# Performance work log

Measured on AMD Instinct MI355X. Metric: run time of the kernel, lower is better.

The kernel has to match this reference:

```python
import jax, jax.numpy as jnp
import numpy as np

N = 50000   # nodes
E = 800000  # edges
F = 128     # n_features
H = 128     # n_hidden
LN_EPS = 1e-5


def setup_inputs() -> dict:
    key = jax.random.key(0)
    ks = jax.random.split(key, 11)
    s = 0.05
    return {
        "x": jax.random.normal(ks[0], (N, F), jnp.float32),
        "edge_index": jax.random.randint(ks[1], (2, E), 0, N, dtype=jnp.int64),
        "edge_attr": jax.random.uniform(ks[2], (E, 1), jnp.float32),
        "ln_gamma": jax.random.normal(ks[3], (F,), jnp.float32),
        "ln_beta": jax.random.normal(ks[4], (F,), jnp.float32),
        "W1": jax.random.normal(ks[5], (F, H), jnp.float32) * s,
        "b1": jax.random.normal(ks[6], (H,), jnp.float32) * s,
        "W2": jax.random.normal(ks[7], (H, H), jnp.float32) * s,
        "b2": jax.random.normal(ks[8], (H,), jnp.float32) * s,
        "W3": jax.random.normal(ks[9], (H, 1), jnp.float32) * s,
        "b3": jax.random.normal(ks[10], (1,), jnp.float32) * s,
    }


def _gcn_conv(x, W, b, row, col, ew, n_nodes):
    """PyG GCNConv: add self loops (weight 1), symmetric normalization,
    gather-scale-scatter aggregation, linear (no bias) + bias."""
    loop = jnp.arange(n_nodes, dtype=row.dtype)
    row_f = jnp.concatenate([row, loop])          # [E+N] source
    col_f = jnp.concatenate([col, loop])          # [E+N] target
    ew_f = jnp.concatenate([ew, jnp.ones((n_nodes,), ew.dtype)])
    deg = jax.ops.segment_sum(ew_f, col_f, num_segments=n_nodes)  # [N]
    dis = jnp.where(deg > 0, jax.lax.rsqrt(jnp.where(deg > 0, deg, 1.0)), 0.0)
    norm = dis[row_f] * ew_f * dis[col_f]          # [E+N]
    h = x @ W                                      # [N, out]
    msg = h[row_f] * norm[:, None]                 # [E+N, out] gather+scale
    out = jax.ops.segment_sum(msg, col_f, num_segments=n_nodes)  # scatter-add
    return out + b


def reference(x, edge_index, edge_attr, ln_gamma, ln_beta, W1, b1, W2, b2, W3, b3):
    x = jnp.nan_to_num(x, nan=0.0, posinf=0.0, neginf=0.0)
    ew = jnp.nan_to_num(edge_attr[:, 0], nan=0.0, posinf=1.0, neginf=0.0)  # [E]
    row, col = edge_index[0], edge_index[1]
    # input LayerNorm
    mu = jnp.mean(x, axis=-1, keepdims=True)
    var = jnp.mean(jnp.square(x - mu), axis=-1, keepdims=True)
    x = (x - mu) * jax.lax.rsqrt(var + LN_EPS) * ln_gamma + ln_beta
    # hidden GCN layers (dropout = identity in eval mode)
    x = jax.nn.relu(_gcn_conv(x, W1, b1, row, col, ew, N))
    x = jax.nn.relu(_gcn_conv(x, W2, b2, row, col, ew, N))
    # output layer
    return _gcn_conv(x, W3, b3, row, col, ew, N)  # [N, 1]
```

## Files before the change

kernel.cpp:

```cpp
#include <hip/hip_runtime.h>
#include <hip/hip_fp16.h>
#include <math.h>

#define NNODES 50000
#define NEDGES 800000
#define NF 128
#define BK 64
#define BINSH 7
#define BINS ((NNODES + 127) >> BINSH)
#define BINCAP 2560
#define EPT 8
#define EPB (1024 * EPT)
constexpr float LN_EPS = 1e-5f;

typedef short v8s __attribute__((ext_vector_type(8)));
typedef unsigned short v8u __attribute__((ext_vector_type(8)));
typedef float v4f __attribute__((ext_vector_type(4)));

__device__ __forceinline__ float clean0(float v) {
    return (isnan(v) || isinf(v)) ? 0.0f : v;
}
__device__ __forceinline__ float cleanw(float v) {
    if (isnan(v)) return 0.0f;
    if (isinf(v)) return v > 0.0f ? 1.0f : 0.0f;
    return v;
}
__device__ __forceinline__ int clampN(int v) {
    return min(max(v, 0), NNODES - 1);
}
__device__ __forceinline__ int pad8(int v) { return (v + 7) & ~7; }

__device__ __forceinline__ unsigned short f2bf(float f) {
    unsigned int u = __float_as_uint(f);
    return (unsigned short)((u + 0x7FFFu + ((u >> 16) & 1u)) >> 16);
}
__device__ __forceinline__ float bf2f(unsigned short h) {
    return __uint_as_float(((unsigned int)h) << 16);
}
__device__ __forceinline__ void split_bf(float v, unsigned short& h, unsigned short& l) {
    h = f2bf(v);
    l = f2bf(v - bf2f(h));
}

__global__ __launch_bounds__(1024) void k_bin_ln(
        const int* __restrict__ ei, const float* __restrict__ ea,
        int* __restrict__ gbin, int2* __restrict__ binned,
        const float* __restrict__ x, const float* __restrict__ gamma,
        const float* __restrict__ beta, unsigned short* __restrict__ z,
        int nbe) {
    if ((int)blockIdx.x < nbe) {
        __shared__ int lcnt[BINS];
        __shared__ int lbase[BINS];
        for (int i = threadIdx.x; i < BINS; i += 1024) lcnt[i] = 0;
        __syncthreads();
        int e0 = blockIdx.x * EPB + threadIdx.x;
        int   myb[EPT]; int myr[EPT]; int mysrc[EPT]; float myw[EPT];
        #pragma unroll
        for (int j = 0; j < EPT; j++) {
            int e = e0 + j * 1024;
            myb[j] = -1;
            if (e < NEDGES) {
                int r = clampN(ei[e]);
                int c = clampN(ei[NEDGES + e]);
                float w = cleanw(ea[e]);
                int b = c >> BINSH;
                myb[j] = b;
                mysrc[j] = ((c & 127) << 16) | r;
                myw[j] = w;
                myr[j] = atomicAdd(&lcnt[b], 1);
            }
        }
        __syncthreads();
        for (int i = threadIdx.x; i < BINS; i += 1024)
            if (lcnt[i] > 0) lbase[i] = atomicAdd(&gbin[i], lcnt[i]);
        __syncthreads();
        #pragma unroll
        for (int j = 0; j < EPT; j++) {
            if (myb[j] >= 0) {
                int pos = lbase[myb[j]] + myr[j];
                if (pos < BINCAP)
                    binned[(size_t)myb[j] * BINCAP + pos] =
                        make_int2(mysrc[j], __float_as_int(myw[j]));
            }
        }
    } else {
        int bid = blockIdx.x - nbe;
        int n = (bid * 1024 + threadIdx.x) >> 6;
        int lane = threadIdx.x & 63;
        if (n >= NNODES) return;
        float2 v = ((const float2*)(x + (size_t)n * NF))[lane];
        v.x = clean0(v.x); v.y = clean0(v.y);
        float s = v.x + v.y;
        for (int o = 32; o > 0; o >>= 1) s += __shfl_xor(s, o);
        float mu = s * (1.0f / NF);
        float dx = v.x - mu, dy = v.y - mu;
        float q = dx * dx + dy * dy;
        for (int o = 32; o > 0; o >>= 1) q += __shfl_xor(q, o);
        float rstd = rsqrtf(q * (1.0f / NF) + LN_EPS);
        float2 g = ((const float2*)gamma)[lane];
        float b = ((const float2*)beta)[lane].x;
        float b2v = ((const float2*)beta)[lane].y;
        float ox = dx * rstd * g.x + b;
        float oy = dy * rstd * g.y + b2v;
        ((__half2*)z)[(size_t)n * 64 + lane] = __float22half2_rn(make_float2(ox, oy));
    }
}

__global__ __launch_bounds__(1024) void k_bucketize(
        const int2* __restrict__ binned, const int* __restrict__ gbin,
        int2* __restrict__ bucket, int* __restrict__ cnt, float* __restrict__ dis,
        const float* __restrict__ W1, const float* __restrict__ W2,
        unsigned short* __restrict__ Wh1T, unsigned short* __restrict__ Wl1T,
        unsigned short* __restrict__ Wh2T, unsigned short* __restrict__ Wl2T,
        int nbb) {
    if ((int)blockIdx.x < nbb) {
        __shared__ int   lc[128];
        __shared__ float ld[128];
        int b = blockIdx.x;
        if (threadIdx.x < 128) { lc[threadIdx.x] = 0; ld[threadIdx.x] = 1.0f; }
        __syncthreads();
        int tot = min(gbin[b], BINCAP);
        const int2* src = binned + (size_t)b * BINCAP;
        for (int i = threadIdx.x; i < tot; i += 1024) {
            int2 rec = src[i];
            int dlo = (rec.x >> 16) & 127;
            int s = rec.x & 0xFFFF;
            int pos = atomicAdd(&lc[dlo], 1);
            int n = (b << BINSH) + dlo;
            if (pos < BK) bucket[(n << 6) + pos] = make_int2(s, rec.y);
            atomicAdd(&ld[dlo], __int_as_float(rec.y));
        }
        __syncthreads();
        if (threadIdx.x < 128) {
            int n = (b << BINSH) + threadIdx.x;
            if (n < NNODES) {
                int c = min(lc[threadIdx.x], BK);
                int cp = pad8(c);
                int beg = n << 6;
                for (int p = beg + c; p < beg + cp; p++) bucket[p] = make_int2(0, 0);
                cnt[n] = cp;
                dis[n] = rsqrtf(ld[threadIdx.x]);
            }
        }
    } else {
        int idx = (blockIdx.x - nbb) * 1024 + threadIdx.x;
        int m = idx >> 14;
        int n = (idx >> 7) & 127;
        int k = idx & 127;
        const float* W = m ? W2 : W1;
        unsigned short* Wh = m ? Wh2T : Wh1T;
        unsigned short* Wl = m ? Wl2T : Wl1T;
        unsigned short h, l;
        split_bf(W[k * 128 + n], h, l);
        Wh[n * 128 + k] = h;
        Wl[n * 128 + k] = l;
    }
}

__global__ __launch_bounds__(256) void k_gemm_mfma(
        const unsigned short* __restrict__ Ain,
        const unsigned short* __restrict__ BhT, const unsigned short* __restrict__ BlT,
        const float* __restrict__ dis, unsigned short* __restrict__ C) {
    int w = threadIdx.x >> 6;
    int lane = threadIdx.x & 63;
    int m = lane & 15;
    int q = lane >> 4;
    int rowbase = blockIdx.x * 64 + w * 16;
    int arow = min(rowbase + m, NNODES - 1);

    const v8u* ap = (const v8u*)(Ain + (size_t)arow * NF);
    v8s afh[4], afl[4];
    #pragma unroll
    for (int c = 0; c < 4; c++) {
        v8u a = ap[c * 4 + q];
        #pragma unroll
        for (int j = 0; j < 8; j++) {
            float f = __half2float(__ushort_as_half(a[j]));
            unsigned short hh, ll;
            split_bf(f, hh, ll);
            afh[c][j] = (short)hh;
            afl[c][j] = (short)ll;
        }
    }

    float ds[4];
    #pragma unroll
    for (int r = 0; r < 4; r++) ds[r] = dis[min(rowbase + q * 4 + r, NNODES - 1)];

    for (int nt = 0; nt < 8; nt++) {
        int n0 = nt * 16;
        const v8s* bhp = (const v8s*)(BhT + (size_t)(n0 + m) * NF);
        const v8s* blp = (const v8s*)(BlT + (size_t)(n0 + m) * NF);
        v4f acc = {0.f, 0.f, 0.f, 0.f};
        #pragma unroll
        for (int c = 0; c < 4; c++) {
            v8s bh = bhp[c * 4 + q];
            v8s bl = blp[c * 4 + q];
            acc = __builtin_amdgcn_mfma_f32_16x16x32_bf16(afh[c], bh, acc, 0, 0, 0);
            acc = __builtin_amdgcn_mfma_f32_16x16x32_bf16(afh[c], bl, acc, 0, 0, 0);
            acc = __builtin_amdgcn_mfma_f32_16x16x32_bf16(afl[c], bh, acc, 0, 0, 0);
        }
        #pragma unroll
        for (int r = 0; r < 4; r++) {
            int gr = rowbase + q * 4 + r;
            if (gr < NNODES)
                C[(size_t)gr * NF + n0 + m] = __half_as_ushort(__float2half(acc[r] * ds[r]));
        }
    }
}

template <bool LAST>
__global__ __launch_bounds__(256) void k_aggregate(
        const unsigned short* __restrict__ h, const float* __restrict__ dis,
        const int* __restrict__ cntp, const int2* __restrict__ bucket,
        const float* __restrict__ bias, unsigned short* __restrict__ y,
        const float* __restrict__ W3, float* __restrict__ h3) {
    int n0 = (blockIdx.x * blockDim.x + threadIdx.x) >> 6;
    if (n0 >= NNODES) return;
    int n = __builtin_amdgcn_readfirstlane(n0);
    int lane = threadIdx.x & 63;
    const __half2* hp = (const __half2*)h;
    float2 acc = __half22float2(hp[(size_t)n * 64 + lane]);
    int beg = n << 6;
    int end = beg + cntp[n];
    int p = beg;
    if (p < end) {
        int2 rec[8];
        #pragma unroll
        for (int j = 0; j < 8; j++) rec[j] = bucket[p + j];
        p += 8;
        while (p < end) {
            float2 v[8];
            #pragma unroll
            for (int j = 0; j < 8; j++) v[j] = __half22float2(hp[(size_t)rec[j].x * 64 + lane]);
            int2 rec2[8];
            #pragma unroll
            for (int j = 0; j < 8; j++) rec2[j] = bucket[p + j];
            #pragma unroll
            for (int j = 0; j < 8; j++) {
                float w = __int_as_float(rec[j].y);
                acc.x += v[j].x * w;
                acc.y += v[j].y * w;
            }
            #pragma unroll
            for (int j = 0; j < 8; j++) rec[j] = rec2[j];
            p += 8;
        }
        float2 v[8];
        #pragma unroll
        for (int j = 0; j < 8; j++) v[j] = __half22float2(hp[(size_t)rec[j].x * 64 + lane]);
        #pragma unroll
        for (int j = 0; j < 8; j++) {
            float w = __int_as_float(rec[j].y);
            acc.x += v[j].x * w;
            acc.y += v[j].y * w;
        }
    }
    float dn = dis[n];
    float2 b = ((const float2*)bias)[lane];
    float ox = fmaxf(acc.x * dn + b.x, 0.0f);
    float oy = fmaxf(acc.y * dn + b.y, 0.0f);
    if (LAST) {
        float2 w3 = ((const float2*)W3)[lane];
        float s = ox * w3.x + oy * w3.y;
        for (int o = 32; o > 0; o >>= 1) s += __shfl_xor(s, o);
        if (lane == 0) h3[n] = s * dn;
    } else {
        ((__half2*)y)[(size_t)n * 64 + lane] = __float22half2_rn(make_float2(ox, oy));
    }
}

__global__ void k_agg_scalar(const float* __restrict__ h3, const float* __restrict__ dis,
                             const int* __restrict__ cntp, const int2* __restrict__ bucket,
                             const float* __restrict__ b3, float* __restrict__ out) {
    int n = blockIdx.x * blockDim.x + threadIdx.x;
    if (n >= NNODES) return;
    float acc = h3[n];
    int beg = n << 6;
    int end = beg + cntp[n];
    for (int p = beg; p + 4 <= end; p += 4) {
        int2 e0 = bucket[p], e1 = bucket[p + 1], e2 = bucket[p + 2], e3 = bucket[p + 3];
        float v0 = h3[e0.x], v1 = h3[e1.x], v2 = h3[e2.x], v3 = h3[e3.x];
        acc += v0 * __int_as_float(e0.y) + v1 * __int_as_float(e1.y)
             + v2 * __int_as_float(e2.y) + v3 * __int_as_float(e3.y);
    }
    out[n] = acc * dis[n] + b3[0];
}

extern "C" void kernel_launch(void* const* d_in, const int* in_sizes, int n_in,
                              void* d_out, int out_size, void* d_ws, size_t ws_size,
                              hipStream_t stream) {
    const float* x  = (const float*)d_in[0];
    const int*   ei = (const int*)d_in[1];
    const float* ea = (const float*)d_in[2];
    const float* g  = (const float*)d_in[3];
    const float* be = (const float*)d_in[4];
    const float* W1 = (const float*)d_in[5];
    const float* b1 = (const float*)d_in[6];
    const float* W2 = (const float*)d_in[7];
    const float* b2 = (const float*)d_in[8];
    const float* W3 = (const float*)d_in[9];
    const float* b3 = (const float*)d_in[10];
    float* out = (float*)d_out;

    char* ws = (char*)d_ws;
    size_t off = 0;
    auto alloc = [&](size_t bytes) {
        void* p = ws + off;
        off += (bytes + 255) & ~((size_t)255);
        return p;
    };
    unsigned short* zbuf = (unsigned short*)alloc((size_t)NNODES * NF * 2);
    unsigned short* hbuf = (unsigned short*)alloc((size_t)NNODES * NF * 2);
    float* dis    = (float*)alloc((size_t)NNODES * 4);
    int*   cnt    = (int*)  alloc((size_t)NNODES * 4);
    int2*  bucket = (int2*) alloc((size_t)NNODES * BK * 8);
    float* h3     = (float*)alloc((size_t)NNODES * 4);
    unsigned short* Wh1T = (unsigned short*)alloc(128 * 128 * 2);
    unsigned short* Wl1T = (unsigned short*)alloc(128 * 128 * 2);
    unsigned short* Wh2T = (unsigned short*)alloc(128 * 128 * 2);
    unsigned short* Wl2T = (unsigned short*)alloc(128 * 128 * 2);
    int*  gbin   = (int*) alloc((size_t)BINS * 4);
    int2* binned = (int2*)alloc((size_t)BINS * BINCAP * 8);
    (void)ws_size; (void)in_sizes; (void)n_in; (void)out_size;

    const int NB_N  = (NNODES + 255) / 256;
    const int NB_W  = (NNODES * 64 + 255) / 256;
    const int NB_G  = (NNODES + 63) / 64;
    const int NBE   = (NEDGES + EPB - 1) / EPB;
    const int NB_LN = NNODES * 64 / 1024;

    hipMemsetAsync(gbin, 0, (size_t)BINS * 4, stream);
    k_bin_ln<<<NBE + NB_LN, 1024, 0, stream>>>(ei, ea, gbin, binned,
                                               x, g, be, zbuf, NBE);
    k_bucketize<<<BINS + 32, 1024, 0, stream>>>(binned, gbin, bucket, cnt, dis,
                                                W1, W2, Wh1T, Wl1T, Wh2T, Wl2T, BINS);

    k_gemm_mfma<<<NB_G, 256, 0, stream>>>(zbuf, Wh1T, Wl1T, dis, hbuf);
    k_aggregate<false><<<NB_W, 256, 0, stream>>>(hbuf, dis, cnt, bucket, b1, zbuf,
                                                 nullptr, nullptr);
    k_gemm_mfma<<<NB_G, 256, 0, stream>>>(zbuf, Wh2T, Wl2T, dis, hbuf);
    k_aggregate<true><<<NB_W, 256, 0, stream>>>(hbuf, dis, cnt, bucket, b2, nullptr,
                                                W3, h3);
    k_agg_scalar<<<NB_N, 256, 0, stream>>>(h3, dis, cnt, bucket, b3, out);
}
```

Baseline: 252.5 us.

## Use fp16 MFMA GEMM and split each wave across two edges in aggregation

The GEMM stops converting the fp16 activations into split bf16 hi/lo pairs. It now feeds fp16 A directly into fp16 MFMA against fp16 hi/lo weight splits, which drops from three MFMAs per k-chunk to two and removes the per-element conversion work. The aggregation kernel now has each half-wave handle a different edge, with each lane loading 8 bytes (4 halves) instead of 4. The two halves are combined with a cross-lane shuffle at the end, which widens memory transactions and halves the serial edge loop. The trade-off is lower A precision in the GEMM (fp16 only, no lo part) and extra shuffle and reduction work in aggregation.

```diff
diff --git a/kernel.cpp b/kernel.cpp
--- a/kernel.cpp
+++ b/kernel.cpp
@@ -13,8 +13,7 @@
 #define EPB (1024 * EPT)
 constexpr float LN_EPS = 1e-5f;
 
-typedef short v8s __attribute__((ext_vector_type(8)));
-typedef unsigned short v8u __attribute__((ext_vector_type(8)));
+typedef _Float16 v8h __attribute__((ext_vector_type(8)));
 typedef float v4f __attribute__((ext_vector_type(4)));
 
 __device__ __forceinline__ float clean0(float v) {
@@ -30,16 +29,13 @@
 }
 __device__ __forceinline__ int pad8(int v) { return (v + 7) & ~7; }
 
-__device__ __forceinline__ unsigned short f2bf(float f) {
-    unsigned int u = __float_as_uint(f);
-    return (unsigned short)((u + 0x7FFFu + ((u >> 16) & 1u)) >> 16);
-}
-__device__ __forceinline__ float bf2f(unsigned short h) {
-    return __uint_as_float(((unsigned int)h) << 16);
-}
-__device__ __forceinline__ void split_bf(float v, unsigned short& h, unsigned short& l) {
-    h = f2bf(v);
-    l = f2bf(v - bf2f(h));
+__device__ __forceinline__ float2 h2f(unsigned int u) {
+    __half2 h = *reinterpret_cast<__half2*>(&u);
+    return __half22float2(h);
+}
+__device__ __forceinline__ unsigned int f2h2(float a, float b) {
+    __half2 h = __float22half2_rn(make_float2(a, b));
+    return *reinterpret_cast<unsigned int*>(&h);
 }
 
 __global__ __launch_bounds__(1024) void k_bin_ln(
@@ -98,11 +94,10 @@
         for (int o = 32; o > 0; o >>= 1) q += __shfl_xor(q, o);
         float rstd = rsqrtf(q * (1.0f / NF) + LN_EPS);
         float2 g = ((const float2*)gamma)[lane];
-        float b = ((const float2*)beta)[lane].x;
-        float b2v = ((const float2*)beta)[lane].y;
-        float ox = dx * rstd * g.x + b;
-        float oy = dy * rstd * g.y + b2v;
-        ((__half2*)z)[(size_t)n * 64 + lane] = __float22half2_rn(make_float2(ox, oy));
+        float2 bb = ((const float2*)beta)[lane];
+        float ox = dx * rstd * g.x + bb.x;
+        float oy = dy * rstd * g.y + bb.y;
+        ((unsigned int*)z)[(size_t)n * 64 + lane] = f2h2(ox, oy);
     }
 }
 
@@ -150,10 +145,11 @@
         const float* W = m ? W2 : W1;
         unsigned short* Wh = m ? Wh2T : Wh1T;
         unsigned short* Wl = m ? Wl2T : Wl1T;
-        unsigned short h, l;
-        split_bf(W[k * 128 + n], h, l);
-        Wh[n * 128 + k] = h;
-        Wl[n * 128 + k] = l;
+        float w = W[k * 128 + n];
+        __half hh = __float2half(w);
+        __half ll = __float2half(w - __half2float(hh));
+        Wh[n * 128 + k] = __half_as_ushort(hh);
+        Wl[n * 128 + k] = __half_as_ushort(ll);
     }
 }
 
@@ -168,20 +164,10 @@
     int rowbase = blockIdx.x * 64 + w * 16;
     int arow = min(rowbase + m, NNODES - 1);
 
-    const v8u* ap = (const v8u*)(Ain + (size_t)arow * NF);
-    v8s afh[4], afl[4];
+    const v8h* ap = (const v8h*)(Ain + (size_t)arow * NF);
+    v8h af[4];
     #pragma unroll
-    for (int c = 0; c < 4; c++) {
-        v8u a = ap[c * 4 + q];
-        #pragma unroll
-        for (int j = 0; j < 8; j++) {
-            float f = __half2float(__ushort_as_half(a[j]));
-            unsigned short hh, ll;
-            split_bf(f, hh, ll);
-            afh[c][j] = (short)hh;
-            afl[c][j] = (short)ll;
-        }
-    }
+    for (int c = 0; c < 4; c++) af[c] = ap[c * 4 + q];
 
     float ds[4];
     #pragma unroll
@@ -189,16 +175,15 @@
 
     for (int nt = 0; nt < 8; nt++) {
         int n0 = nt * 16;
-        const v8s* bhp = (const v8s*)(BhT + (size_t)(n0 + m) * NF);
-        const v8s* blp = (const v8s*)(BlT + (size_t)(n0 + m) * NF);
+        const v8h* bhp = (const v8h*)(BhT + (size_t)(n0 + m) * NF);
+        const v8h* blp = (const v8h*)(BlT + (size_t)(n0 + m) * NF);
         v4f acc = {0.f, 0.f, 0.f, 0.f};
         #pragma unroll
         for (int c = 0; c < 4; c++) {
-            v8s bh = bhp[c * 4 + q];
-            v8s bl = blp[c * 4 + q];
-            acc = __builtin_amdgcn_mfma_f32_16x16x32_bf16(afh[c], bh, acc, 0, 0, 0);
-            acc = __builtin_amdgcn_mfma_f32_16x16x32_bf16(afh[c], bl, acc, 0, 0, 0);
-            acc = __builtin_amdgcn_mfma_f32_16x16x32_bf16(afl[c], bh, acc, 0, 0, 0);
+            v8h bh = bhp[c * 4 + q];
+            v8h bl = blp[c * 4 + q];
+            acc = __builtin_amdgcn_mfma_f32_16x16x32_f16(af[c], bh, acc, 0, 0, 0);
+            acc = __builtin_amdgcn_mfma_f32_16x16x32_f16(af[c], bl, acc, 0, 0, 0);
         }
         #pragma unroll
         for (int r = 0; r < 4; r++) {
@@ -219,54 +204,75 @@
     if (n0 >= NNODES) return;
     int n = __builtin_amdgcn_readfirstlane(n0);
     int lane = threadIdx.x & 63;
-    const __half2* hp = (const __half2*)h;
-    float2 acc = __half22float2(hp[(size_t)n * 64 + lane]);
+    int lo = lane & 31;
+    int hi = lane >> 5;
+    const uint2* hp2 = (const uint2*)h;
+    float4 acc = {0.f, 0.f, 0.f, 0.f};
+    {
+        uint2 sv = hp2[(size_t)n * 32 + lo];
+        if (hi == 0) {
+            float2 f0 = h2f(sv.x), f1 = h2f(sv.y);
+            acc.x = f0.x; acc.y = f0.y; acc.z = f1.x; acc.w = f1.y;
+        }
+    }
     int beg = n << 6;
     int end = beg + cntp[n];
     int p = beg;
     if (p < end) {
-        int2 rec[8];
-        #pragma unroll
-        for (int j = 0; j < 8; j++) rec[j] = bucket[p + j];
+        int2 rec[4];
+        #pragma unroll
+        for (int j = 0; j < 4; j++) rec[j] = bucket[p + 2 * j + hi];
         p += 8;
         while (p < end) {
-            float2 v[8];
+            uint2 v[4];
             #pragma unroll
-            for (int j = 0; j < 8; j++) v[j] = __half22float2(hp[(size_t)rec[j].x * 64 + lane]);
-            int2 rec2[8];
+            for (int j = 0; j < 4; j++) v[j] = hp2[(size_t)rec[j].x * 32 + lo];
+            int2 rec2[4];
             #pragma unroll
-            for (int j = 0; j < 8; j++) rec2[j] = bucket[p + j];
+            for (int j = 0; j < 4; j++) rec2[j] = bucket[p + 2 * j + hi];
             #pragma unroll
-            for (int j = 0; j < 8; j++) {
-                float w = __int_as_float(rec[j].y);
-                acc.x += v[j].x * w;
-                acc.y += v[j].y * w;
+            for (int j = 0; j < 4; j++) {
+                float wv = __int_as_float(rec[j].y);
+                float2 f0 = h2f(v[j].x), f1 = h2f(v[j].y);
+                acc.x += f0.x * wv; acc.y += f0.y * wv;
+                acc.z += f1.x * wv; acc.w += f1.y * wv;
             }
             #pragma unroll
-            for (int j = 0; j < 8; j++) rec[j] = rec2[j];
+            for (int j = 0; j < 4; j++) rec[j] = rec2[j];
             p += 8;
         }
-        float2 v[8];
-        #pragma unroll
-        for (int j = 0; j < 8; j++) v[j] = __half22float2(hp[(size_t)rec[j].x * 64 + lane]);
-        #pragma unroll
-        for (int j = 0; j < 8; j++) {
-            float w = __int_as_float(rec[j].y);
-            acc.x += v[j].x * w;
-            acc.y += v[j].y * w;
-        }
-    }
+        uint2 v[4];
+        #pragma unroll
+        for (int j = 0; j < 4; j++) v[j] = hp2[(size_t)rec[j].x * 32 + lo];
+        #pragma unroll
+        for (int j = 0; j < 4; j++) {
+            float wv = __int_as_float(rec[j].y);
+            float2 f0 = h2f(v[j].x), f1 = h2f(v[j].y);
+            acc.x += f0.x * wv; acc.y += f0.y * wv;
+            acc.z += f1.x * wv; acc.w += f1.y * wv;
+        }
+    }
+    acc.x += __shfl_xor(acc.x, 32);
+    acc.y += __shfl_xor(acc.y, 32);
+    acc.z += __shfl_xor(acc.z, 32);
+    acc.w += __shfl_xor(acc.w, 32);
+
     float dn = dis[n];
-    float2 b = ((const float2*)bias)[lane];
-    float ox = fmaxf(acc.x * dn + b.x, 0.0f);
-    float oy = fmaxf(acc.y * dn + b.y, 0.0f);
+    float4 b = ((const float4*)bias)[lo];
+    float o0 = fmaxf(acc.x * dn + b.x, 0.0f);
+    float o1 = fmaxf(acc.y * dn + b.y, 0.0f);
+    float o2 = fmaxf(acc.z * dn + b.z, 0.0f);
+    float o3 = fmaxf(acc.w * dn + b.w, 0.0f);
     if (LAST) {
-        float2 w3 = ((const float2*)W3)[lane];
-        float s = ox * w3.x + oy * w3.y;
-        for (int o = 32; o > 0; o >>= 1) s += __shfl_xor(s, o);
+        float4 w3 = ((const float4*)W3)[lo];
+        float s = o0 * w3.x + o1 * w3.y + o2 * w3.z + o3 * w3.w;
+        for (int o = 16; o > 0; o >>= 1) s += __shfl_xor(s, o);
         if (lane == 0) h3[n] = s * dn;
-    } else {
-        ((__half2*)y)[(size_t)n * 64 + lane] = __float22half2_rn(make_float2(ox, oy));
+    } else if (hi == 0) {
+        uint2 pv;
+        pv.x = f2h2(o0, o1);
+        pv.y = f2h2(o2, o3);
+        ((uint2*)y)[(size_t)n * 32 + lo] = pv;
     }
 }
 
```

Result: slower. 264.1 us (+4.6%).
